# Kernel optimization log

Measured on AMD Instinct MI355X. Metric: run time of the kernel, lower is better.

## Reference

```python
import jax, jax.numpy as jnp
import numpy as np

IN_F = 4096
OUT_F = 4096
BATCH = 1024

def setup_inputs() -> dict:
    key = jax.random.key(0)
    k = jax.random.split(key, 7)
    x = jax.random.normal(k[0], (BATCH, IN_F), dtype=jnp.float32)
    weight_mu = jax.random.normal(k[1], (OUT_F, IN_F), dtype=jnp.float32) * (1.0 / np.sqrt(IN_F))
    # torch init: uniform(-5,-3) for sigma params (raw values, used directly as std)
    weight_sigma = jax.random.uniform(k[2], (OUT_F, IN_F), dtype=jnp.float32, minval=-5.0, maxval=-3.0)
    bias_mu = jnp.zeros((OUT_F,), dtype=jnp.float32)
    bias_sigma = jax.random.uniform(k[3], (OUT_F,), dtype=jnp.float32, minval=-5.0, maxval=-3.0)
    eps_w = jax.random.normal(k[4], (OUT_F, IN_F), dtype=jnp.float32)
    eps_b = jax.random.normal(k[5], (OUT_F,), dtype=jnp.float32)
    return {"x": x, "weight_mu": weight_mu, "weight_sigma": weight_sigma,
            "bias_mu": bias_mu, "bias_sigma": bias_sigma,
            "eps_w": eps_w, "eps_b": eps_b}

def reference(x, weight_mu, weight_sigma, bias_mu, bias_sigma, eps_w, eps_b):
    # training-mode forward: reparameterized weight sample then dense matmul
    weight = weight_mu + eps_w * weight_sigma        # [out, in]
    bias = bias_mu + eps_b * bias_sigma              # [out]
    # F.linear(x, W, b) = x @ W.T + b
    return jnp.einsum('bi,oi->bo', x, weight) + bias
```

## Files before the change

kernel.cpp:

```cpp
#include <hip/hip_runtime.h>
#include <hip/hip_bf16.h>
#include <stdint.h>

#define M_BATCH 1024
#define N_OUT   4096
#define K_IN    4096

#define BM 128
#define BN 128
#define BK 64
#define KPER  (K_IN / 2)
#define KITER (KPER / BK)

typedef __attribute__((ext_vector_type(8))) __bf16 bf16x8_t;
typedef __attribute__((ext_vector_type(4))) float f32x4_t;
typedef __attribute__((ext_vector_type(4))) float fvec4;
typedef __attribute__((ext_vector_type(4))) unsigned short us4_t;

__device__ __forceinline__ unsigned short f2bf_bits(float f) {
    union { __hip_bfloat16 h; unsigned short u; } cvt;
    cvt.h = __float2bfloat16(f);
    return cvt.u;
}

__global__ __launch_bounds__(256) void prep_kernel(
    const float* __restrict__ x,
    const float* __restrict__ wmu,
    const float* __restrict__ wsig,
    const float* __restrict__ epsw,
    unsigned short* __restrict__ wb,
    unsigned short* __restrict__ xb)
{
    const size_t tid = (size_t)blockIdx.x * blockDim.x + threadIdx.x;
    const size_t T   = (size_t)1048576;

    const fvec4* wmu4  = (const fvec4*)wmu;
    const fvec4* wsig4 = (const fvec4*)wsig;
    const fvec4* epsw4 = (const fvec4*)epsw;
    us4_t* wb4 = (us4_t*)wb;

    fvec4 m[4], s[4], e[4];
    #pragma unroll
    for (int r = 0; r < 4; ++r) {
        const size_t i = tid + (size_t)r * T;
        m[r] = __builtin_nontemporal_load(wmu4  + i);
        s[r] = __builtin_nontemporal_load(wsig4 + i);
        e[r] = __builtin_nontemporal_load(epsw4 + i);
    }
    #pragma unroll
    for (int r = 0; r < 4; ++r) {
        us4_t o;
        o.x = f2bf_bits(fmaf(e[r].x, s[r].x, m[r].x));
        o.y = f2bf_bits(fmaf(e[r].y, s[r].y, m[r].y));
        o.z = f2bf_bits(fmaf(e[r].z, s[r].z, m[r].z));
        o.w = f2bf_bits(fmaf(e[r].w, s[r].w, m[r].w));
        __builtin_nontemporal_store(o, wb4 + (tid + (size_t)r * T));
    }

    fvec4 v = __builtin_nontemporal_load((const fvec4*)x + tid);
    us4_t o;
    o.x = f2bf_bits(v.x);
    o.y = f2bf_bits(v.y);
    o.z = f2bf_bits(v.z);
    o.w = f2bf_bits(v.w);
    __builtin_nontemporal_store(o, (us4_t*)xb + tid);
}

__global__ __launch_bounds__(512, 2) void gemm_bt_kernel(
    const unsigned short* __restrict__ A,
    const unsigned short* __restrict__ B,
    const float* __restrict__ bmu,
    const float* __restrict__ bsig,
    const float* __restrict__ ebias,
    float* __restrict__ C)
{
    __shared__ unsigned short lds[2 * 32768];

    const int t   = threadIdx.x;
    const int b   = blockIdx.x;
    const int bn  = (b & 7) | (((b >> 3) & 3) << 3);
    const int bm  = b >> 5;
    const int bm0 = bm * BM;
    const int bn0 = bn * BN;
    const int lane  = t & 63;
    const int wave  = t >> 6;
    const int khalf = wave >> 2;
    const int quadw = wave & 3;
    const int wrow  = (quadw >> 1) * 64;
    const int wcol  = (quadw & 1) * 64;
    const int lm    = lane & 15;
    const int quad  = lane >> 4;

    f32x4_t acc[4][4] = {};

    const unsigned short* srcs[8];
    const int rlow = t >> 3;
    const int jsw  = ((t & 7) ^ (rlow & 7)) * 8;
    #pragma unroll
    for (int s = 0; s < 8; ++s) {
        const int row  = rlow + (s & 1) * 64;
        const int half = (s >> 1) & 1;
        const unsigned short* base = (s < 4)
            ? (A + (size_t)(bm0 + row) * K_IN)
            : (B + (size_t)(bn0 + row) * K_IN);
        srcs[s] = base + half * KPER + jsw;
    }
    char* dst0 = (char*)lds + t * 16;

    #pragma unroll
    for (int s = 0; s < 8; ++s)
        __builtin_amdgcn_global_load_lds(
            (const __attribute__((address_space(1))) void*)(srcs[s]),
            (__attribute__((address_space(3))) void*)(dst0 + s * 8192), 16, 0, 0);

    for (int it = 0; it < KITER; ++it) {
        __syncthreads();

        if (it + 1 < KITER) {
            const int koff = (it + 1) * BK;
            const int nb   = ((it + 1) & 1) * 65536;
            #pragma unroll
            for (int s = 0; s < 8; ++s)
                __builtin_amdgcn_global_load_lds(
                    (const __attribute__((address_space(1))) void*)(srcs[s] + koff),
                    (__attribute__((address_space(3))) void*)(dst0 + nb + s * 8192), 16, 0, 0);
        }

        const unsigned short* Lb = lds + (it & 1) * 32768;
        const unsigned short* Ah = Lb + khalf * 8192;
        const unsigned short* Bh = Lb + 16384 + khalf * 8192;

        #pragma unroll
        for (int kk = 0; kk < 2; ++kk) {
            const int p = ((kk * 4) + quad) ^ (lm & 7);
            bf16x8_t a_frag[4], b_frag[4];
            #pragma unroll
            for (int im = 0; im < 4; im++)
                a_frag[im] = *(const bf16x8_t*)(Ah + ((wrow + im * 16 + lm) * 8 + p) * 8);
            #pragma unroll
            for (int jn = 0; jn < 4; jn++)
                b_frag[jn] = *(const bf16x8_t*)(Bh + ((wcol + jn * 16 + lm) * 8 + p) * 8);
            #pragma unroll
            for (int im = 0; im < 4; im++)
                #pragma unroll
                for (int jn = 0; jn < 4; jn++)
                    acc[im][jn] = __builtin_amdgcn_mfma_f32_16x16x32_bf16(
                        a_frag[im], b_frag[jn], acc[im][jn], 0, 0, 0);
        }
    }

    f32x4_t* red = (f32x4_t*)lds;
    if (wave >= 4) {
        #pragma unroll
        for (int im = 0; im < 4; im++)
            #pragma unroll
            for (int jn = 0; jn < 4; jn++)
                red[quadw * 1024 + (im * 4 + jn) * 64 + lane] = acc[im][jn];
    }
    __syncthreads();
    if (wave < 4) {
        #pragma unroll
        for (int jn = 0; jn < 4; jn++) {
            const int gn = bn0 + wcol + jn * 16 + lm;
            const float bias = bmu[gn] + ebias[gn] * bsig[gn];
            #pragma unroll
            for (int im = 0; im < 4; im++) {
                const f32x4_t part = red[quadw * 1024 + (im * 4 + jn) * 64 + lane];
                const int gm0 = bm0 + wrow + im * 16 + quad * 4;
                #pragma unroll
                for (int r = 0; r < 4; r++)
                    C[(size_t)(gm0 + r) * N_OUT + gn] = acc[im][jn][r] + part[r] + bias;
            }
        }
    }
}

__global__ __launch_bounds__(256) void naive_kernel(
    const float* __restrict__ x, const float* __restrict__ wmu,
    const float* __restrict__ wsig, const float* __restrict__ bmu,
    const float* __restrict__ bsig, const float* __restrict__ epsw,
    const float* __restrict__ epsb, float* __restrict__ out)
{
    const int o = blockIdx.x * blockDim.x + threadIdx.x;
    const int b = blockIdx.y;
    const float4* xr = (const float4*)(x + (size_t)b * K_IN);
    const float4* mr = (const float4*)(wmu + (size_t)o * K_IN);
    const float4* sr = (const float4*)(wsig + (size_t)o * K_IN);
    const float4* er = (const float4*)(epsw + (size_t)o * K_IN);
    float s = 0.f;
    for (int k = 0; k < K_IN / 4; k++) {
        float4 xv = xr[k], m = mr[k], sg = sr[k], e = er[k];
        s += xv.x * fmaf(e.x, sg.x, m.x);
        s += xv.y * fmaf(e.y, sg.y, m.y);
        s += xv.z * fmaf(e.z, sg.z, m.z);
        s += xv.w * fmaf(e.w, sg.w, m.w);
    }
    out[(size_t)b * N_OUT + o] = s + bmu[o] + epsb[o] * bsig[o];
}

extern "C" void kernel_launch(void* const* d_in, const int* in_sizes, int n_in,
                              void* d_out, int out_size, void* d_ws, size_t ws_size,
                              hipStream_t stream)
{
    const float* x    = (const float*)d_in[0];
    const float* wmu  = (const float*)d_in[1];
    const float* wsig = (const float*)d_in[2];
    const float* bmu  = (const float*)d_in[3];
    const float* bsig = (const float*)d_in[4];
    const float* epsw = (const float*)d_in[5];
    const float* epsb = (const float*)d_in[6];
    float* out = (float*)d_out;

    const size_t need = ((size_t)N_OUT * K_IN + (size_t)M_BATCH * K_IN) * sizeof(unsigned short);
    if (ws_size >= need) {
        unsigned short* wb = (unsigned short*)d_ws;
        unsigned short* xb = wb + (size_t)N_OUT * K_IN;
        prep_kernel<<<4096, 256, 0, stream>>>(x, wmu, wsig, epsw, wb, xb);
        gemm_bt_kernel<<<256, 512, 0, stream>>>(xb, wb, bmu, bsig, epsb, out);
    } else {
        dim3 grid(N_OUT / 256, M_BATCH);
        naive_kernel<<<grid, 256, 0, stream>>>(x, wmu, wsig, bmu, bsig, epsw, epsb, out);
    }
}
```

Baseline: 254.3 us.

## Deepen GEMM LDS pipeline to four stages with smaller K tiles and vmcnt waits

Reworks the GEMM main loop from a double-buffered BK=64 scheme into a four-buffer BK=32 pipeline with three tiles in flight, using explicit s_waitcnt vmcnt plus s_barrier instead of __syncthreads. The goal is to keep more global-to-LDS loads outstanding and hide memory latency behind MFMA work. The LDS swizzle is changed to match the 32-wide K rows. The prep kernel's nontemporal stores also become regular stores, so the bf16 operands may stay in cache for the GEMM. In exchange there are more barriers per unit of K, and correctness depends on the hand-counted vmcnt values.

```diff
diff --git a/kernel.cpp b/kernel.cpp
--- a/kernel.cpp
+++ b/kernel.cpp
@@ -8,9 +8,9 @@
 
 #define BM 128
 #define BN 128
-#define BK 64
-#define KPER  (K_IN / 2)
-#define KITER (KPER / BK)
+#define KPER   (K_IN / 2)
+#define BK2    32
+#define KITER2 (KPER / BK2)
 
 typedef __attribute__((ext_vector_type(8))) __bf16 bf16x8_t;
 typedef __attribute__((ext_vector_type(4))) float f32x4_t;
@@ -54,7 +54,7 @@
         o.y = f2bf_bits(fmaf(e[r].y, s[r].y, m[r].y));
         o.z = f2bf_bits(fmaf(e[r].z, s[r].z, m[r].z));
         o.w = f2bf_bits(fmaf(e[r].w, s[r].w, m[r].w));
-        __builtin_nontemporal_store(o, wb4 + (tid + (size_t)r * T));
+        wb4[tid + (size_t)r * T] = o;
     }
 
     fvec4 v = __builtin_nontemporal_load((const fvec4*)x + tid);
@@ -63,7 +63,7 @@
     o.y = f2bf_bits(v.y);
     o.z = f2bf_bits(v.z);
     o.w = f2bf_bits(v.w);
-    __builtin_nontemporal_store(o, (us4_t*)xb + tid);
+    ((us4_t*)xb)[tid] = o;
 }
 
 __global__ __launch_bounds__(512, 2) void gemm_bt_kernel(
@@ -74,7 +74,7 @@
     const float* __restrict__ ebias,
     float* __restrict__ C)
 {
-    __shared__ unsigned short lds[2 * 32768];
+    __shared__ unsigned short lds[4 * 16384];
 
     const int t   = threadIdx.x;
     const int b   = blockIdx.x;
@@ -90,64 +90,62 @@
     const int wcol  = (quadw & 1) * 64;
     const int lm    = lane & 15;
     const int quad  = lane >> 4;
+    const int fq    = quad ^ ((lm >> 1) & 3);
 
     f32x4_t acc[4][4] = {};
 
-    const unsigned short* srcs[8];
-    const int rlow = t >> 3;
-    const int jsw  = ((t & 7) ^ (rlow & 7)) * 8;
-    #pragma unroll
-    for (int s = 0; s < 8; ++s) {
-        const int row  = rlow + (s & 1) * 64;
-        const int half = (s >> 1) & 1;
-        const unsigned short* base = (s < 4)
-            ? (A + (size_t)(bm0 + row) * K_IN)
-            : (B + (size_t)(bn0 + row) * K_IN);
-        srcs[s] = base + half * KPER + jsw;
-    }
-    char* dst0 = (char*)lds + t * 16;
-
-    #pragma unroll
-    for (int s = 0; s < 8; ++s)
-        __builtin_amdgcn_global_load_lds(
-            (const __attribute__((address_space(1))) void*)(srcs[s]),
-            (__attribute__((address_space(3))) void*)(dst0 + s * 8192), 16, 0, 0);
-
-    for (int it = 0; it < KITER; ++it) {
-        __syncthreads();
-
-        if (it + 1 < KITER) {
-            const int koff = (it + 1) * BK;
-            const int nb   = ((it + 1) & 1) * 65536;
-            #pragma unroll
-            for (int s = 0; s < 8; ++s)
-                __builtin_amdgcn_global_load_lds(
-                    (const __attribute__((address_space(1))) void*)(srcs[s] + koff),
-                    (__attribute__((address_space(3))) void*)(dst0 + nb + s * 8192), 16, 0, 0);
-        }
-
-        const unsigned short* Lb = lds + (it & 1) * 32768;
-        const unsigned short* Ah = Lb + khalf * 8192;
-        const unsigned short* Bh = Lb + 16384 + khalf * 8192;
-
-        #pragma unroll
-        for (int kk = 0; kk < 2; ++kk) {
-            const int p = ((kk * 4) + quad) ^ (lm & 7);
-            bf16x8_t a_frag[4], b_frag[4];
-            #pragma unroll
-            for (int im = 0; im < 4; im++)
-                a_frag[im] = *(const bf16x8_t*)(Ah + ((wrow + im * 16 + lm) * 8 + p) * 8);
+    const int row   = t >> 2;
+    const int chlog = (t & 3) ^ ((t >> 3) & 3);
+    const unsigned short* srcs[4];
+    srcs[0] = A + (size_t)(bm0 + row) * K_IN + chlog * 8;
+    srcs[1] = srcs[0] + KPER;
+    srcs[2] = B + (size_t)(bn0 + row) * K_IN + chlog * 8;
+    srcs[3] = srcs[2] + KPER;
+    char* dstt = (char*)lds + t * 16;
+
+    auto STAGE = [&](int it) {
+        const int koff = it * BK2;
+        char* d = dstt + (it & 3) * 32768;
+        #pragma unroll
+        for (int s = 0; s < 4; ++s)
+            __builtin_amdgcn_global_load_lds(
+                (const __attribute__((address_space(1))) void*)(srcs[s] + koff),
+                (__attribute__((address_space(3))) void*)(d + s * 8192), 16, 0, 0);
+    };
+
+    auto COMPUTE = [&](int it) {
+        const unsigned short* Lb = lds + (it & 3) * 16384;
+        const unsigned short* Ah = Lb + khalf * 4096 + (wrow + lm) * 32 + fq * 8;
+        const unsigned short* Bh = Lb + 8192 + khalf * 4096 + (wcol + lm) * 32 + fq * 8;
+        bf16x8_t a_frag[4], b_frag[4];
+        #pragma unroll
+        for (int im = 0; im < 4; im++)
+            a_frag[im] = *(const bf16x8_t*)(Ah + im * 512);
+        #pragma unroll
+        for (int jn = 0; jn < 4; jn++)
+            b_frag[jn] = *(const bf16x8_t*)(Bh + jn * 512);
+        #pragma unroll
+        for (int im = 0; im < 4; im++)
             #pragma unroll
             for (int jn = 0; jn < 4; jn++)
-                b_frag[jn] = *(const bf16x8_t*)(Bh + ((wcol + jn * 16 + lm) * 8 + p) * 8);
-            #pragma unroll
-            for (int im = 0; im < 4; im++)
-                #pragma unroll
-                for (int jn = 0; jn < 4; jn++)
-                    acc[im][jn] = __builtin_amdgcn_mfma_f32_16x16x32_bf16(
-                        a_frag[im], b_frag[jn], acc[im][jn], 0, 0, 0);
-        }
-    }
+                acc[im][jn] = __builtin_amdgcn_mfma_f32_16x16x32_bf16(
+                    a_frag[im], b_frag[jn], acc[im][jn], 0, 0, 0);
+        __builtin_amdgcn_sched_barrier(0);
+    };
+
+    STAGE(0); STAGE(1); STAGE(2);
+
+    for (int it = 0; it < KITER2 - 3; ++it) {
+        asm volatile("s_waitcnt vmcnt(8)\n\ts_barrier" ::: "memory");
+        STAGE(it + 3);
+        COMPUTE(it);
+    }
+    asm volatile("s_waitcnt vmcnt(8)\n\ts_barrier" ::: "memory");
+    COMPUTE(KITER2 - 3);
+    asm volatile("s_waitcnt vmcnt(4)\n\ts_barrier" ::: "memory");
+    COMPUTE(KITER2 - 2);
+    asm volatile("s_waitcnt vmcnt(0)\n\ts_barrier" ::: "memory");
+    COMPUTE(KITER2 - 1);
 
     f32x4_t* red = (f32x4_t*)lds;
     if (wave >= 4) {
```

After: 246.1 us. -3.2%, faster.
